# Kernel optimization log

Measured on AMD Instinct MI355X. Metric: run time of the kernel, lower is better.

The kernel has to match this reference:

```python
import jax, jax.numpy as jnp
import numpy as np

V, D, H, L, T_MAX = 50257, 1024, 16, 12, 256
HS = D // H
B, T = 8, 256


def setup_inputs() -> dict:
    key = jax.random.key(0)
    ks = jax.random.split(key, 24)
    s = 0.02
    inp = {
        'idx': jax.random.randint(ks[0], (B, T), 0, V),
        'targets': jax.random.randint(ks[1], (B, T), 0, V),
        'tok_emb': jax.random.normal(ks[2], (V, D), jnp.float32) * s,
        'pos_emb': jax.random.normal(ks[3], (T_MAX, D), jnp.float32) * s,
        'Wq': jax.random.normal(ks[4], (L, H, D, HS), jnp.float32) / np.sqrt(D),
        'Wk': jax.random.normal(ks[5], (L, H, D, HS), jnp.float32) / np.sqrt(D),
        'Wv': jax.random.normal(ks[6], (L, H, D, HS), jnp.float32) / np.sqrt(D),
        'ln1_g': jnp.ones((L, D), jnp.float32),
        'ln1_b': jnp.zeros((L, D), jnp.float32),
        'ln2_g': jnp.ones((L, D), jnp.float32),
        'ln2_b': jnp.zeros((L, D), jnp.float32),
        'fc1_w': jax.random.normal(ks[7], (L, D, 4 * D), jnp.float32) / np.sqrt(D),
        'fc1_b': jnp.zeros((L, 4 * D), jnp.float32),
        'fc2_w': jax.random.normal(ks[8], (L, 4 * D, D), jnp.float32) / np.sqrt(4 * D),
        'fc2_b': jnp.zeros((L, D), jnp.float32),
        'lnf_g': jnp.ones((D,), jnp.float32),
        'lnf_b': jnp.zeros((D,), jnp.float32),
        'lm_w': jax.random.normal(ks[9], (D, V), jnp.float32) / np.sqrt(D),
        'lm_b': jnp.zeros((V,), jnp.float32),
    }
    return inp


def _layernorm(x, g, b, eps=1e-5):
    mu = jnp.mean(x, axis=-1, keepdims=True)
    var = jnp.var(x, axis=-1, keepdims=True)
    return (x - mu) * jax.lax.rsqrt(var + eps) * g + b


def reference(idx, targets, tok_emb, pos_emb, Wq, Wk, Wv, ln1_g, ln1_b, ln2_g, ln2_b,
              fc1_w, fc1_b, fc2_w, fc2_b, lnf_g, lnf_b, lm_w, lm_b):
    Bc, Tc = idx.shape
    x = tok_emb[idx] + pos_emb[:Tc]  # [B,T,D]
    causal = jnp.tril(jnp.ones((Tc, Tc), bool))
    scale = 1.0 / np.sqrt(HS)
    for l in range(L):
        h = _layernorm(x, ln1_g[l], ln1_b[l])
        q = jnp.einsum('btd,hds->bhts', h, Wq[l])
        k = jnp.einsum('btd,hds->bhts', h, Wk[l])
        v = jnp.einsum('btd,hds->bhts', h, Wv[l])
        scores = jnp.einsum('bhts,bhus->bhtu', q, k) * scale
        scores = jnp.where(causal, scores, -jnp.inf)
        attn = jax.nn.softmax(scores, axis=-1)
        o = jnp.einsum('bhtu,bhus->bhts', attn, v)  # [B,H,T,hs]
        o = o.transpose(0, 2, 1, 3).reshape(Bc, Tc, D)  # concat heads
        x = x + o  # no output projection in original
        h = _layernorm(x, ln2_g[l], ln2_b[l])
        ff = jax.nn.relu(h @ fc1_w[l] + fc1_b[l]) @ fc2_w[l] + fc2_b[l]
        x = x + ff
    x = _layernorm(x, lnf_g, lnf_b)
    logits = x @ lm_w + lm_b  # [B,T,V]
    logp = jax.nn.log_softmax(logits, axis=-1)
    nll = -jnp.take_along_axis(logp, targets[..., None], axis=-1)[..., 0]
    loss = jnp.mean(nll)
    return logits, loss
```

## Files before the change

### kernel.cpp

```cpp
#include <hip/hip_runtime.h>

#define T_SEQ 256
#define DMODEL 1024
#define NHEAD 16
#define HSZ 64
#define NLAYER 12
#define VOCAB 50257
#define NPAD 50304
#define FF 4096
#define MROWS 2048

using short8 = __attribute__((ext_vector_type(8))) short;
using f32x4  = __attribute__((ext_vector_type(4))) float;

__device__ __forceinline__ float bf2f(unsigned short u) {
    unsigned int x = ((unsigned int)u) << 16;
    return __builtin_bit_cast(float, x);
}
__device__ __forceinline__ unsigned short f2bf(float f) {
    unsigned int u = __builtin_bit_cast(unsigned int, f);
    unsigned int r = (u + 0x7fffu + ((u >> 16) & 1u)) >> 16;
    return (unsigned short)r;
}
__device__ __forceinline__ void async_copy16(const void* g, void* l) {
    __builtin_amdgcn_global_load_lds(
        (const __attribute__((address_space(1))) unsigned int*)g,
        (__attribute__((address_space(3))) unsigned int*)l, 16, 0, 0);
}

__device__ __forceinline__ void ln_tail(
    float4 v, const float* __restrict__ g, const float* __restrict__ b,
    int row, int tid, unsigned short* __restrict__ out)
{
    float s  = v.x + v.y + v.z + v.w;
    float ss = v.x * v.x + v.y * v.y + v.z * v.z + v.w * v.w;
    for (int o = 32; o > 0; o >>= 1) {
        s  += __shfl_down(s, o);
        ss += __shfl_down(ss, o);
    }
    __shared__ float ps[4], pss[4];
    int wave = tid >> 6, lane = tid & 63;
    if (lane == 0) { ps[wave] = s; pss[wave] = ss; }
    __syncthreads();
    float st  = ps[0] + ps[1] + ps[2] + ps[3];
    float sst = pss[0] + pss[1] + pss[2] + pss[3];
    float mu  = st * (1.0f / DMODEL);
    float var = sst * (1.0f / DMODEL) - mu * mu;
    float rstd = rsqrtf(var + 1e-5f);
    float4 gv = ((const float4*)g)[tid];
    float4 bv = ((const float4*)b)[tid];
    ushort4 o4;
    o4.x = f2bf((v.x - mu) * rstd * gv.x + bv.x);
    o4.y = f2bf((v.y - mu) * rstd * gv.y + bv.y);
    o4.z = f2bf((v.z - mu) * rstd * gv.z + bv.z);
    o4.w = f2bf((v.w - mu) * rstd * gv.w + bv.w);
    ((ushort4*)out)[(size_t)row * (DMODEL / 4) + tid] = o4;
}

__global__ __launch_bounds__(256) void embed_ln_kernel(
    const int* __restrict__ idx, const float* __restrict__ tok,
    const float* __restrict__ pos, const float* __restrict__ g,
    const float* __restrict__ b, float* __restrict__ x,
    unsigned short* __restrict__ h)
{
    int row = blockIdx.x, tid = threadIdx.x;
    int t = row & (T_SEQ - 1);
    int token = idx[row];
    float4 a = ((const float4*)(tok + (size_t)token * DMODEL))[tid];
    float4 p = ((const float4*)(pos + (size_t)t * DMODEL))[tid];
    float4 v;
    v.x = a.x + p.x; v.y = a.y + p.y; v.z = a.z + p.z; v.w = a.w + p.w;
    ((float4*)(x + (size_t)row * DMODEL))[tid] = v;
    ln_tail(v, g, b, row, tid, h);
}

__global__ __launch_bounds__(256) void ln_kernel(
    const float* __restrict__ x, const float* __restrict__ g,
    const float* __restrict__ b, unsigned short* __restrict__ out)
{
    int row = blockIdx.x, tid = threadIdx.x;
    float4 v = ((const float4*)(x + (size_t)row * DMODEL))[tid];
    ln_tail(v, g, b, row, tid, out);
}

__global__ __launch_bounds__(256) void fc2_merge_ln_kernel(
    const float* __restrict__ part, const float* __restrict__ bias,
    const float* __restrict__ g, const float* __restrict__ b,
    float* __restrict__ x, unsigned short* __restrict__ h)
{
    int row = blockIdx.x, tid = threadIdx.x;
    size_t o = (size_t)row * (DMODEL / 4) + tid;
    float4 p0 = ((const float4*)part)[o];
    float4 p1 = ((const float4*)part)[o + MROWS * (DMODEL / 4)];
    float4 bv = ((const float4*)bias)[tid];
    float4 v = ((float4*)x)[o];
    v.x += p0.x + p1.x + bv.x;
    v.y += p0.y + p1.y + bv.y;
    v.z += p0.z + p1.z + bv.z;
    v.w += p0.w + p1.w + bv.w;
    ((float4*)x)[o] = v;
    ln_tail(v, g, b, row, tid, h);
}

__global__ __launch_bounds__(256) void wtranspose64_kernel(
    const float* __restrict__ in, unsigned short* __restrict__ out,
    int R, int C, long in_l, long out_l)
{
    int lyr = blockIdx.z;
    in  += (size_t)lyr * in_l;
    out += (size_t)lyr * out_l;
    __shared__ float tile[64][65];
    int tx = threadIdx.x & 15, ty = threadIdx.x >> 4;
    int c0 = blockIdx.x * 64, r0 = blockIdx.y * 64;
    #pragma unroll
    for (int i = 0; i < 4; i++) {
        int r = ty + i * 16;
        int c = tx * 4;
        int gc = c0 + c;
        const float* src = in + (size_t)(r0 + r) * C + gc;
        float4 v;
        if (gc + 3 < C) {
            v = *(const float4*)src;
        } else {
            v.x = (gc     < C) ? src[0] : 0.f;
            v.y = (gc + 1 < C) ? src[1] : 0.f;
            v.z = (gc + 2 < C) ? src[2] : 0.f;
            v.w = (gc + 3 < C) ? src[3] : 0.f;
        }
        tile[r][c] = v.x; tile[r][c + 1] = v.y;
        tile[r][c + 2] = v.z; tile[r][c + 3] = v.w;
    }
    __syncthreads();
    int sr = (threadIdx.x & 7) * 8;
    int scb = threadIdx.x >> 3;
    #pragma unroll
    for (int i = 0; i < 2; i++) {
        int c = scb + i * 32;
        unsigned short w[8];
        #pragma unroll
        for (int j = 0; j < 8; j++) w[j] = f2bf(tile[sr + j][c]);
        *(short8*)(void*)(out + (size_t)(c0 + c) * R + r0 + sr) = *(short8*)(void*)w;
    }
}

__global__ __launch_bounds__(256) void qkvpack64_kernel(
    const float* __restrict__ Wq, const float* __restrict__ Wk,
    const float* __restrict__ Wv, unsigned short* __restrict__ out,
    long w_l, long out_l)
{
    int z = blockIdx.z;
    int lyr = z / 48, r48 = z % 48;
    int seg = r48 >> 4, hh = r48 & 15;
    const float* W = (seg == 0 ? Wq : seg == 1 ? Wk : Wv)
                     + (size_t)lyr * w_l + (size_t)hh * DMODEL * HSZ;
    unsigned short* o = out + (size_t)lyr * out_l
                      + (size_t)(seg * 1024 + hh * 64) * DMODEL;
    __shared__ float tile[64][65];
    int tx = threadIdx.x & 15, ty = threadIdx.x >> 4;
    int d0 = blockIdx.x * 64;
    #pragma unroll
    for (int i = 0; i < 4; i++) {
        int d = ty + i * 16;
        float4 v = *(const float4*)(W + (size_t)(d0 + d) * HSZ + tx * 4);
        tile[d][tx * 4] = v.x; tile[d][tx * 4 + 1] = v.y;
        tile[d][tx * 4 + 2] = v.z; tile[d][tx * 4 + 3] = v.w;
    }
    __syncthreads();
    int db = (threadIdx.x & 7) * 8;
    int sb = threadIdx.x >> 3;
    #pragma unroll
    for (int i = 0; i < 2; i++) {
        int s = sb + i * 32;
        unsigned short w[8];
        #pragma unroll
        for (int j = 0; j < 8; j++) w[j] = f2bf(tile[db + j][s]);
        *(short8*)(void*)(o + (size_t)s * DMODEL + d0 + db) = *(short8*)(void*)w;
    }
}

template<int MF, int WAVES, int WCOLS, bool QKV, bool RELU, bool RES, bool CBF16>
__device__ __forceinline__ void gemm_core(
    const unsigned short* __restrict__ A, int lda,
    const unsigned short* __restrict__ Bt, int ldb,
    const float* __restrict__ bias,
    void* __restrict__ Cv, int ldc,
    const float* __restrict__ res, int ldr,
    int N, int K,
    unsigned short* __restrict__ vtout)
{
    constexpr int BM = MF * 16 * (WAVES / WCOLS);
    constexpr int BN = 64 * WCOLS;
    constexpr int AJ = (BM * 8) / (WAVES * 64);
    constexpr int BJ = (BN * 8) / (WAVES * 64);
    __shared__ __align__(16) char As[BM * 128];
    __shared__ __align__(16) char Bs[BN * 128];
    int tid = threadIdx.x;
    int wave = tid >> 6, lane = tid & 63;
    int wr = wave / WCOLS, wc = wave % WCOLS;
    int m0 = blockIdx.x * BM, n0 = blockIdx.y * BN;

    f32x4 acc[MF][4];
    #pragma unroll
    for (int m = 0; m < MF; m++)
        #pragma unroll
        for (int n = 0; n < 4; n++)
            acc[m][n] = (f32x4){0.f, 0.f, 0.f, 0.f};

    int ksw = (((lane & 7) ^ (lane >> 3)) << 4);
    int KT = K >> 6;
    for (int kt = 0; kt < KT; kt++) {
        int k0 = kt << 6;
        __syncthreads();
        #pragma unroll
        for (int j = 0; j < AJ; j++) {
            int row = (wave * AJ + j) * 8 + (lane >> 3);
            const char* src = (const char*)A + ((size_t)(m0 + row) * lda + k0) * 2 + ksw;
            async_copy16(src, As + (wave * AJ + j) * 1024);
        }
        #pragma unroll
        for (int j = 0; j < BJ; j++) {
            int nrow = (wave * BJ + j) * 8 + (lane >> 3);
            const char* src = (const char*)Bt + ((size_t)(n0 + nrow) * ldb + k0) * 2 + ksw;
            async_copy16(src, Bs + (wave * BJ + j) * 1024);
        }
        __syncthreads();
        #pragma unroll
        for (int ks = 0; ks < 2; ks++) {
            int kb = ks * 64 + ((lane >> 4) << 4);
            short8 a[MF], b[4];
            #pragma unroll
            for (int m = 0; m < MF; m++) {
                int r = wr * (MF * 16) + m * 16 + (lane & 15);
                a[m] = *(const short8*)(const void*)(As + r * 128 + (kb ^ ((r & 7) << 4)));
            }
            #pragma unroll
            for (int n = 0; n < 4; n++) {
                int c = wc * 64 + n * 16 + (lane & 15);
                b[n] = *(const short8*)(const void*)(Bs + c * 128 + (kb ^ ((c & 7) << 4)));
            }
            #pragma unroll
            for (int m = 0; m < MF; m++)
                #pragma unroll
                for (int n = 0; n < 4; n++)
                    acc[m][n] = __builtin_amdgcn_mfma_f32_16x16x32_bf16(a[m], b[n], acc[m][n], 0, 0, 0);
        }
    }
    #pragma unroll
    for (int m = 0; m < MF; m++) {
        int rowb = m0 + wr * (MF * 16) + m * 16 + ((lane >> 4) << 2);
        #pragma unroll
        for (int n = 0; n < 4; n++) {
            int col = n0 + wc * 64 + n * 16 + (lane & 15);
            if (col < N) {
                float bi = bias ? bias[col] : 0.f;
                #pragma unroll
                for (int r2 = 0; r2 < 4; r2++) {
                    float v = acc[m][n][r2] + bi;
                    if (RELU) v = fmaxf(v, 0.f);
                    int row = rowb + r2;
                    if (RES) v += res[(size_t)row * ldr + col];
                    if (QKV && col >= 2048) {
                        int hh = (col - 2048) >> 6, sdim = (col - 2048) & 63;
                        int bb = row >> 8, tt = row & 255;
                        vtout[((((size_t)bb * NHEAD + hh) * HSZ + sdim) * T_SEQ) + tt] = f2bf(v);
                    } else if (CBF16) {
                        ((unsigned short*)Cv)[(size_t)row * ldc + col] = f2bf(v);
                    } else {
                        ((float*)Cv)[(size_t)row * ldc + col] = v;
                    }
                }
            }
        }
    }
}

__global__ __launch_bounds__(256) void gemm_qkv(
    const unsigned short* __restrict__ A, const unsigned short* __restrict__ Bt,
    unsigned short* __restrict__ C, unsigned short* __restrict__ vtout)
{
    gemm_core<4, 4, 2, true, false, false, true>(
        A, DMODEL, Bt, DMODEL, nullptr, C, 3072, nullptr, 0, 3072, DMODEL, vtout);
}

__global__ __launch_bounds__(256) void gemm_fc1(
    const unsigned short* __restrict__ A, const unsigned short* __restrict__ Bt,
    const float* __restrict__ bias, unsigned short* __restrict__ C)
{
    gemm_core<4, 4, 2, false, true, false, true>(
        A, DMODEL, Bt, DMODEL, bias, C, FF, nullptr, 0, FF, DMODEL, nullptr);
}

__global__ __launch_bounds__(256) void gemm_fc2(
    const unsigned short* __restrict__ A, const unsigned short* __restrict__ Bt,
    float* __restrict__ part)
{
    int z = blockIdx.z;
    gemm_core<2, 4, 2, false, false, false, false>(
        A + z * 2048, FF, Bt + z * 2048, FF, nullptr,
        part + (size_t)z * MROWS * DMODEL, DMODEL, nullptr, 0,
        DMODEL, 2048, nullptr);
}

__global__ __launch_bounds__(512) void gemm_lm(
    const unsigned short* __restrict__ A, const unsigned short* __restrict__ Bt,
    const float* __restrict__ bias, float* __restrict__ C)
{
    gemm_core<4, 8, 2, false, false, false, false>(
        A, DMODEL, Bt, DMODEL, bias, C, VOCAB, nullptr, 0, VOCAB, DMODEL, nullptr);
}

__global__ __launch_bounds__(256) void attn_fused_kernel(
    const unsigned short* __restrict__ qkv, const unsigned short* __restrict__ vt,
    float* __restrict__ x)
{
    int qt = blockIdx.x, hh = blockIdx.y, b = blockIdx.z;
    int tid = threadIdx.x;
    int wave = tid >> 6, lane = tid & 63;
    int g = lane >> 4, q = lane & 15;

    __shared__ __align__(16) char Kb[4][8192];
    __shared__ __align__(16) char Vb[4][8192];
    __shared__ __align__(16) char Plds[4][2048];

    int qrow = b * T_SEQ + qt * 64 + wave * 16 + q;
    const char* qp = (const char*)qkv + ((size_t)qrow * 3072 + hh * HSZ) * 2;
    short8 qreg[2];
    qreg[0] = *(const short8*)(const void*)(qp + (g << 4));
    qreg[1] = *(const short8*)(const void*)(qp + 64 + (g << 4));

    char* Pw = Plds[wave];

    f32x4 oacc[4];
    #pragma unroll
    for (int f = 0; f < 4; f++) oacc[f] = (f32x4){0.f, 0.f, 0.f, 0.f};
    float m_run = -1e30f, l_run = 0.f;

    int srow = wave * 8 + (lane >> 3);
    int sbyte = ((lane & 7) << 4) ^ ((srow & 7) << 4);

    for (int kt = 0; kt <= qt; kt++) {
        #pragma unroll
        for (int c = 0; c < 2; c++) {
            int row = c * 32 + srow;
            const char* src = (const char*)qkv +
                ((size_t)(b * T_SEQ + kt * 64 + row) * 3072 + 1024 + hh * HSZ) * 2 + sbyte;
            async_copy16(src, Kb[kt] + c * 4096 + wave * 1024);
        }
        #pragma unroll
        for (int c = 0; c < 2; c++) {
            int row = c * 32 + srow;
            const char* src = (const char*)vt +
                (((size_t)(b * NHEAD + hh) * HSZ + row) * T_SEQ + kt * 64) * 2 + sbyte;
            async_copy16(src, Vb[kt] + c * 4096 + wave * 1024);
        }
    }
    __syncthreads();

    for (int kt = 0; kt <= qt; kt++) {
        f32x4 sacc[4];
        #pragma unroll
        for (int f = 0; f < 4; f++) sacc[f] = (f32x4){0.f, 0.f, 0.f, 0.f};
        #pragma unroll
        for (int ks = 0; ks < 2; ks++) {
            int kb = ks * 64 + (g << 4);
            #pragma unroll
            for (int f = 0; f < 4; f++) {
                int u = f * 16 + q;
                short8 kf = *(const short8*)(const void*)(Kb[kt] + u * 128 + (kb ^ ((u & 7) << 4)));
                sacc[f] = __builtin_amdgcn_mfma_f32_16x16x32_bf16(kf, qreg[ks], sacc[f], 0, 0, 0);
            }
        }
        float sv[4][4];
        #pragma unroll
        for (int f = 0; f < 4; f++)
            #pragma unroll
            for (int r = 0; r < 4; r++) {
                float v = sacc[f][r] * 0.125f;
                if (kt == qt) {
                    int u_loc = f * 16 + g * 4 + r;
                    if (u_loc > wave * 16 + q) v = -1e30f;
                }
                sv[f][r] = v;
            }
        float pm = -1e30f;
        #pragma unroll
        for (int f = 0; f < 4; f++)
            #pragma unroll
            for (int r = 0; r < 4; r++) pm = fmaxf(pm, sv[f][r]);
        pm = fmaxf(pm, __shfl_xor(pm, 16));
        pm = fmaxf(pm, __shfl_xor(pm, 32));
        float mnew = fmaxf(m_run, pm);
        float corr = __expf(m_run - mnew);
        float p[4][4];
        float ls = 0.f;
        #pragma unroll
        for (int f = 0; f < 4; f++)
            #pragma unroll
            for (int r = 0; r < 4; r++) {
                p[f][r] = __expf(sv[f][r] - mnew);
                ls += p[f][r];
            }
        ls += __shfl_xor(ls, 16);
        ls += __shfl_xor(ls, 32);
        l_run = l_run * corr + ls;
        m_run = mnew;
        #pragma unroll
        for (int r = 0; r < 4; r++) {
            float cr = __shfl(corr, (lane & 48) | (g * 4 + r));
            #pragma unroll
            for (int f = 0; f < 4; f++) oacc[f][r] *= cr;
        }
        #pragma unroll
        for (int f = 0; f < 4; f++)
            #pragma unroll
            for (int rp = 0; rp < 2; rp++) {
                int ue = f * 16 + g * 4 + rp * 2;
                unsigned int pk = (unsigned int)f2bf(p[f][rp * 2])
                                | ((unsigned int)f2bf(p[f][rp * 2 + 1]) << 16);
                *(unsigned int*)(void*)(Pw + q * 128 + ((ue * 2) ^ ((q & 7) << 4))) = pk;
            }
        #pragma unroll
        for (int ks = 0; ks < 2; ks++) {
            int kb = ks * 64 + (g << 4);
            short8 pa = *(const short8*)(const void*)(Pw + q * 128 + (kb ^ ((q & 7) << 4)));
            #pragma unroll
            for (int f = 0; f < 4; f++) {
                int s = f * 16 + q;
                short8 vf = *(const short8*)(const void*)(Vb[kt] + s * 128 + (kb ^ ((s & 7) << 4)));
                oacc[f] = __builtin_amdgcn_mfma_f32_16x16x32_bf16(pa, vf, oacc[f], 0, 0, 0);
            }
        }
    }
    float inv = 1.0f / l_run;
    #pragma unroll
    for (int r = 0; r < 4; r++) {
        float ir = __shfl(inv, (lane & 48) | (g * 4 + r));
        int row_g = b * T_SEQ + qt * 64 + wave * 16 + g * 4 + r;
        #pragma unroll
        for (int f = 0; f < 4; f++) {
            size_t xi = (size_t)row_g * DMODEL + hh * HSZ + f * 16 + q;
            x[xi] += oacc[f][r] * ir;
        }
    }
}

__global__ __launch_bounds__(512) void loss1_kernel(
    const float* __restrict__ logits, const int* __restrict__ targets,
    float* __restrict__ nll)
{
    int r = blockIdx.x, tid = threadIdx.x;
    const float* row = logits + (size_t)r * VOCAB;
    const float4* row4 = (const float4*)row;
    float m = -3.4e38f, s = 0.f;
    for (int v = tid; v < VOCAB / 4; v += 512) {
        float4 x4 = row4[v];
        float lm = fmaxf(fmaxf(x4.x, x4.y), fmaxf(x4.z, x4.w));
        float nm = fmaxf(m, lm);
        s = s * __expf(m - nm) + __expf(x4.x - nm) + __expf(x4.y - nm)
          + __expf(x4.z - nm) + __expf(x4.w - nm);
        m = nm;
    }
    if (tid == 0) {
        float xv = row[VOCAB - 1];
        float nm = fmaxf(m, xv);
        s = s * __expf(m - nm) + __expf(xv - nm);
        m = nm;
    }
    __shared__ float ms[512], ssh[512];
    ms[tid] = m; ssh[tid] = s;
    __syncthreads();
    for (int o = 256; o > 0; o >>= 1) {
        if (tid < o) {
            float m1 = ms[tid], s1 = ssh[tid];
            float m2 = ms[tid + o], s2 = ssh[tid + o];
            float nm = fmaxf(m1, m2);
            ssh[tid] = s1 * __expf(m1 - nm) + s2 * __expf(m2 - nm);
            ms[tid] = nm;
        }
        __syncthreads();
    }
    if (tid == 0) nll[r] = logf(ssh[0]) + ms[0] - row[targets[r]];
}

__global__ __launch_bounds__(256) void loss2_kernel(
    const float* __restrict__ nll, float* __restrict__ out)
{
    int tid = threadIdx.x;
    float s = 0.f;
    for (int i = tid; i < MROWS; i += 256) s += nll[i];
    __shared__ float red[256];
    red[tid] = s;
    __syncthreads();
    for (int o = 128; o > 0; o >>= 1) {
        if (tid < o) red[tid] += red[tid + o];
        __syncthreads();
    }
    if (tid == 0) out[0] = red[0] * (1.0f / MROWS);
}

extern "C" void kernel_launch(void* const* d_in, const int* in_sizes, int n_in,
                              void* d_out, int out_size, void* d_ws, size_t ws_size,
                              hipStream_t stream)
{
    const int*   idx  = (const int*)d_in[0];
    const int*   tgt  = (const int*)d_in[1];
    const float* tok  = (const float*)d_in[2];
    const float* pos  = (const float*)d_in[3];
    const float* Wq   = (const float*)d_in[4];
    const float* Wk   = (const float*)d_in[5];
    const float* Wv   = (const float*)d_in[6];
    const float* ln1g = (const float*)d_in[7];
    const float* ln1b = (const float*)d_in[8];
    const float* ln2g = (const float*)d_in[9];
    const float* ln2b = (const float*)d_in[10];
    const float* fc1w = (const float*)d_in[11];
    const float* fc1b = (const float*)d_in[12];
    const float* fc2w = (const float*)d_in[13];
    const float* fc2b = (const float*)d_in[14];
    const float* lnfg = (const float*)d_in[15];
    const float* lnfb = (const float*)d_in[16];
    const float* lmw  = (const float*)d_in[17];
    const float* lmb  = (const float*)d_in[18];

    char* ws = (char*)d_ws;
    float*          x    = (float*)(ws + 0);
    unsigned short* h    = (unsigned short*)(ws + 8388608);
    unsigned short* qkv  = (unsigned short*)(ws + 12582912);
    unsigned short* vt   = (unsigned short*)(ws + 25165824);
    unsigned short* mid  = (unsigned short*)(ws + 29360128);
    float*          nll  = (float*)(ws + 46137344);
    float*          fc2p = (float*)(ws + 46145536);
    unsigned short* lmwt = (unsigned short*)(ws + 62922752);
    const size_t UP_NEED = 442769408ull;
    bool upfront = (ws_size >= UP_NEED);
    unsigned short* qkvt = (unsigned short*)(ws + 165945344);
    unsigned short* fc1t, * fc2t;
    long qkvt_l, fc1t_l, fc2t_l;
    if (upfront) {
        fc1t = (unsigned short*)(ws + 241442816);
        fc2t = (unsigned short*)(ws + 342106112);
        qkvt_l = 3072 * 1024; fc1t_l = (long)FF * 1024; fc2t_l = (long)1024 * FF;
    } else {
        fc1t = (unsigned short*)(ws + 172236800);
        fc2t = (unsigned short*)(ws + 180625408);
        qkvt_l = 0; fc1t_l = 0; fc2t_l = 0;
    }
    float* logits = (float*)d_out;
    float* lossp  = logits + (size_t)MROWS * VOCAB;

    const long WQKV_L = (long)NHEAD * DMODEL * HSZ;
    if (upfront) {
        qkvpack64_kernel<<<dim3(16, 1, 48 * NLAYER), 256, 0, stream>>>(
            Wq, Wk, Wv, qkvt, WQKV_L, qkvt_l);
        wtranspose64_kernel<<<dim3(64, 16, NLAYER), 256, 0, stream>>>(
            fc1w, fc1t, DMODEL, FF, (long)DMODEL * FF, fc1t_l);
        wtranspose64_kernel<<<dim3(16, 64, NLAYER), 256, 0, stream>>>(
            fc2w, fc2t, FF, DMODEL, (long)FF * DMODEL, fc2t_l);
    }
    wtranspose64_kernel<<<dim3(786, 16, 1), 256, 0, stream>>>(
        lmw, lmwt, DMODEL, VOCAB, 0, 0);

    embed_ln_kernel<<<MROWS, 256, 0, stream>>>(idx, tok, pos, ln1g, ln1b, x, h);

    for (int l = 0; l < NLAYER; l++) {
        unsigned short* qkvt_p = qkvt + (size_t)l * qkvt_l;
        unsigned short* fc1t_p = fc1t + (size_t)l * fc1t_l;
        unsigned short* fc2t_p = fc2t + (size_t)l * fc2t_l;
        if (!upfront) {
            qkvpack64_kernel<<<dim3(16, 1, 48), 256, 0, stream>>>(
                Wq + (size_t)l * WQKV_L, Wk + (size_t)l * WQKV_L,
                Wv + (size_t)l * WQKV_L, qkvt, WQKV_L, 0);
            wtranspose64_kernel<<<dim3(64, 16, 1), 256, 0, stream>>>(
                fc1w + (size_t)l * DMODEL * FF, fc1t, DMODEL, FF, 0, 0);
            wtranspose64_kernel<<<dim3(16, 64, 1), 256, 0, stream>>>(
                fc2w + (size_t)l * FF * DMODEL, fc2t, FF, DMODEL, 0, 0);
        }
        gemm_qkv<<<dim3(16, 24), 256, 0, stream>>>(h, qkvt_p, qkv, vt);
        attn_fused_kernel<<<dim3(4, NHEAD, 8), 256, 0, stream>>>(qkv, vt, x);
        ln_kernel<<<MROWS, 256, 0, stream>>>(x, ln2g + l * DMODEL, ln2b + l * DMODEL, h);
        gemm_fc1<<<dim3(16, 32), 256, 0, stream>>>(h, fc1t_p, fc1b + (size_t)l * FF, mid);
        gemm_fc2<<<dim3(32, 8, 2), 256, 0, stream>>>(mid, fc2t_p, fc2p);
        const float* ng = (l < NLAYER - 1) ? ln1g + (l + 1) * DMODEL : lnfg;
        const float* nb = (l < NLAYER - 1) ? ln1b + (l + 1) * DMODEL : lnfb;
        fc2_merge_ln_kernel<<<MROWS, 256, 0, stream>>>(
            fc2p, fc2b + (size_t)l * DMODEL, ng, nb, x, h);
    }

    gemm_lm<<<dim3(8, 393), 512, 0, stream>>>(h, lmwt, lmb, logits);

    loss1_kernel<<<MROWS, 512, 0, stream>>>(logits, tgt, nll);
    loss2_kernel<<<1, 256, 0, stream>>>(nll, lossp);
}
```

Measured before the change: 2.090 ms.

## Fuse per-strip log-softmax partials into LM-head GEMM epilogue

The LM-head GEMM epilogue now computes, for each row, a per-64-column-strip max and sum of exponentials using wave shuffles, and writes them to scratch reused from the fc2 partial buffer. The old loss kernel, which re-read the full 2048x50257 logits array, is replaced by a small kernel that merges 786 partials per row and reads only the target logit. This removes about 400MB of logits reads in exchange for extra epilogue shuffles and exp work in the GEMM.

Result: faster. 2.043 ms (-2.2%).

```diff
diff --git a/kernel.cpp b/kernel.cpp
--- a/kernel.cpp
+++ b/kernel.cpp
@@ -9,6 +9,7 @@
 #define NPAD 50304
 #define FF 4096
 #define MROWS 2048
+#define NSTRIPS 786
 
 using short8 = __attribute__((ext_vector_type(8))) short;
 using f32x4  = __attribute__((ext_vector_type(4))) float;
@@ -178,7 +179,7 @@
     }
 }
 
-template<int MF, int WAVES, int WCOLS, bool QKV, bool RELU, bool RES, bool CBF16>
+template<int MF, int WAVES, int WCOLS, bool QKV, bool RELU, bool RES, bool CBF16, bool LOSSP>
 __device__ __forceinline__ void gemm_core(
     const unsigned short* __restrict__ A, int lda,
     const unsigned short* __restrict__ Bt, int ldb,
@@ -186,7 +187,8 @@
     void* __restrict__ Cv, int ldc,
     const float* __restrict__ res, int ldr,
     int N, int K,
-    unsigned short* __restrict__ vtout)
+    unsigned short* __restrict__ vtout,
+    float* __restrict__ pmax, float* __restrict__ psum)
 {
     constexpr int BM = MF * 16 * (WAVES / WCOLS);
     constexpr int BN = 64 * WCOLS;
@@ -248,16 +250,18 @@
     #pragma unroll
     for (int m = 0; m < MF; m++) {
         int rowb = m0 + wr * (MF * 16) + m * 16 + ((lane >> 4) << 2);
+        float val[4][4];
         #pragma unroll
         for (int n = 0; n < 4; n++) {
             int col = n0 + wc * 64 + n * 16 + (lane & 15);
-            if (col < N) {
-                float bi = bias ? bias[col] : 0.f;
-                #pragma unroll
-                for (int r2 = 0; r2 < 4; r2++) {
-                    float v = acc[m][n][r2] + bi;
-                    if (RELU) v = fmaxf(v, 0.f);
-                    int row = rowb + r2;
+            bool okc = (col < N);
+            float bi = (bias && okc) ? bias[col] : 0.f;
+            #pragma unroll
+            for (int r2 = 0; r2 < 4; r2++) {
+                float v = acc[m][n][r2] + bi;
+                if (RELU) v = fmaxf(v, 0.f);
+                int row = rowb + r2;
+                if (okc) {
                     if (RES) v += res[(size_t)row * ldr + col];
                     if (QKV && col >= 2048) {
                         int hh = (col - 2048) >> 6, sdim = (col - 2048) & 63;
@@ -269,6 +273,27 @@
                         ((float*)Cv)[(size_t)row * ldc + col] = v;
                     }
                 }
+                if (LOSSP) val[n][r2] = okc ? v : -1e30f;
+            }
+        }
+        if (LOSSP) {
+            #pragma unroll
+            for (int r2 = 0; r2 < 4; r2++) {
+                float M = fmaxf(fmaxf(val[0][r2], val[1][r2]),
+                                fmaxf(val[2][r2], val[3][r2]));
+                #pragma unroll
+                for (int o = 1; o < 16; o <<= 1) M = fmaxf(M, __shfl_xor(M, o));
+                float S = 0.f;
+                #pragma unroll
+                for (int n = 0; n < 4; n++) S += __expf(val[n][r2] - M);
+                #pragma unroll
+                for (int o = 1; o < 16; o <<= 1) S += __shfl_xor(S, o);
+                if ((lane & 15) == 0) {
+                    int row = rowb + r2;
+                    int strip = blockIdx.y * WCOLS + wc;
+                    pmax[(size_t)row * NSTRIPS + strip] = M;
+                    psum[(size_t)row * NSTRIPS + strip] = S;
+                }
             }
         }
     }
@@ -278,16 +303,18 @@
     const unsigned short* __restrict__ A, const unsigned short* __restrict__ Bt,
     unsigned short* __restrict__ C, unsigned short* __restrict__ vtout)
 {
-    gemm_core<4, 4, 2, true, false, false, true>(
-        A, DMODEL, Bt, DMODEL, nullptr, C, 3072, nullptr, 0, 3072, DMODEL, vtout);
+    gemm_core<4, 4, 2, true, false, false, true, false>(
+        A, DMODEL, Bt, DMODEL, nullptr, C, 3072, nullptr, 0, 3072, DMODEL,
+        vtout, nullptr, nullptr);
 }
 
 __global__ __launch_bounds__(256) void gemm_fc1(
     const unsigned short* __restrict__ A, const unsigned short* __restrict__ Bt,
     const float* __restrict__ bias, unsigned short* __restrict__ C)
 {
-    gemm_core<4, 4, 2, false, true, false, true>(
-        A, DMODEL, Bt, DMODEL, bias, C, FF, nullptr, 0, FF, DMODEL, nullptr);
+    gemm_core<4, 4, 2, false, true, false, true, false>(
+        A, DMODEL, Bt, DMODEL, bias, C, FF, nullptr, 0, FF, DMODEL,
+        nullptr, nullptr, nullptr);
 }
 
 __global__ __launch_bounds__(256) void gemm_fc2(
@@ -295,18 +322,20 @@
     float* __restrict__ part)
 {
     int z = blockIdx.z;
-    gemm_core<2, 4, 2, false, false, false, false>(
+    gemm_core<2, 4, 2, false, false, false, false, false>(
         A + z * 2048, FF, Bt + z * 2048, FF, nullptr,
         part + (size_t)z * MROWS * DMODEL, DMODEL, nullptr, 0,
-        DMODEL, 2048, nullptr);
+        DMODEL, 2048, nullptr, nullptr, nullptr);
 }
 
 __global__ __launch_bounds__(512) void gemm_lm(
     const unsigned short* __restrict__ A, const unsigned short* __restrict__ Bt,
-    const float* __restrict__ bias, float* __restrict__ C)
-{
-    gemm_core<4, 8, 2, false, false, false, false>(
-        A, DMODEL, Bt, DMODEL, bias, C, VOCAB, nullptr, 0, VOCAB, DMODEL, nullptr);
+    const float* __restrict__ bias, float* __restrict__ C,
+    float* __restrict__ pmax, float* __restrict__ psum)
+{
+    gemm_core<4, 8, 2, false, false, false, false, true>(
+        A, DMODEL, Bt, DMODEL, bias, C, VOCAB, nullptr, 0, VOCAB, DMODEL,
+        nullptr, pmax, psum);
 }
 
 __global__ __launch_bounds__(256) void attn_fused_kernel(
@@ -444,42 +473,36 @@
     }
 }
 
-__global__ __launch_bounds__(512) void loss1_kernel(
+__global__ __launch_bounds__(256) void loss_reduce_kernel(
+    const float* __restrict__ pmax, const float* __restrict__ psum,
     const float* __restrict__ logits, const int* __restrict__ targets,
     float* __restrict__ nll)
 {
-    int r = blockIdx.x, tid = threadIdx.x;
-    const float* row = logits + (size_t)r * VOCAB;
-    const float4* row4 = (const float4*)row;
-    float m = -3.4e38f, s = 0.f;
-    for (int v = tid; v < VOCAB / 4; v += 512) {
-        float4 x4 = row4[v];
-        float lm = fmaxf(fmaxf(x4.x, x4.y), fmaxf(x4.z, x4.w));
-        float nm = fmaxf(m, lm);
-        s = s * __expf(m - nm) + __expf(x4.x - nm) + __expf(x4.y - nm)
-          + __expf(x4.z - nm) + __expf(x4.w - nm);
-        m = nm;
-    }
-    if (tid == 0) {
-        float xv = row[VOCAB - 1];
-        float nm = fmaxf(m, xv);
-        s = s * __expf(m - nm) + __expf(xv - nm);
-        m = nm;
-    }
-    __shared__ float ms[512], ssh[512];
-    ms[tid] = m; ssh[tid] = s;
+    int row = blockIdx.x, tid = threadIdx.x;
+    const float* pm = pmax + (size_t)row * NSTRIPS;
+    const float* ps = psum + (size_t)row * NSTRIPS;
+    float M = -1e30f, S = 0.f;
+    for (int i = tid; i < NSTRIPS; i += 256) {
+        float m2 = pm[i], s2 = ps[i];
+        float nm = fmaxf(M, m2);
+        S = S * __expf(M - nm) + s2 * __expf(m2 - nm);
+        M = nm;
+    }
+    __shared__ float Ms[256], Ss[256];
+    Ms[tid] = M; Ss[tid] = S;
     __syncthreads();
-    for (int o = 256; o > 0; o >>= 1) {
+    for (int o = 128; o > 0; o >>= 1) {
         if (tid < o) {
-            float m1 = ms[tid], s1 = ssh[tid];
-            float m2 = ms[tid + o], s2 = ssh[tid + o];
+            float m1 = Ms[tid], s1 = Ss[tid];
+            float m2 = Ms[tid + o], s2 = Ss[tid + o];
             float nm = fmaxf(m1, m2);
-            ssh[tid] = s1 * __expf(m1 - nm) + s2 * __expf(m2 - nm);
-            ms[tid] = nm;
+            Ss[tid] = s1 * __expf(m1 - nm) + s2 * __expf(m2 - nm);
+            Ms[tid] = nm;
         }
         __syncthreads();
     }
-    if (tid == 0) nll[r] = logf(ssh[0]) + ms[0] - row[targets[r]];
+    if (tid == 0)
+        nll[row] = logf(Ss[0]) + Ms[0] - logits[(size_t)row * VOCAB + targets[row]];
 }
 
 __global__ __launch_bounds__(256) void loss2_kernel(
@@ -531,6 +554,8 @@
     float*          nll  = (float*)(ws + 46137344);
     float*          fc2p = (float*)(ws + 46145536);
     unsigned short* lmwt = (unsigned short*)(ws + 62922752);
+    float*          pmax = fc2p;
+    float*          psum = fc2p + (size_t)MROWS * NSTRIPS;
     const size_t UP_NEED = 442769408ull;
     bool upfront = (ws_size >= UP_NEED);
     unsigned short* qkvt = (unsigned short*)(ws + 165945344);
@@ -586,8 +611,8 @@
             fc2p, fc2b + (size_t)l * DMODEL, ng, nb, x, h);
     }
 
-    gemm_lm<<<dim3(8, 393), 512, 0, stream>>>(h, lmwt, lmb, logits);
-
-    loss1_kernel<<<MROWS, 512, 0, stream>>>(logits, tgt, nll);
+    gemm_lm<<<dim3(8, 393), 512, 0, stream>>>(h, lmwt, lmb, logits, pmax, psum);
+
+    loss_reduce_kernel<<<MROWS, 256, 0, stream>>>(pmax, psum, logits, tgt, nll);
     loss2_kernel<<<1, 256, 0, stream>>>(nll, lossp);
 }
```
